# Kernel optimization log

Measured on AMD Instinct MI355X. Metric: run time of the kernel, lower is better.

Reference implementation:

```python
import jax, jax.numpy as jnp
import numpy as np

EPS = 1e-8

@jax.custom_vjp
def spike(x):
    # Heaviside forward, SuperSpike surrogate gradient in backward
    return (x > 0.0).astype(x.dtype)

def _spike_fwd(x):
    return spike(x), x

def _spike_bwd(x, g):
    return (g / (1.0 + 10.0 * jnp.abs(x)) ** 2,)

spike.defvjp(_spike_fwd, _spike_bwd)


def setup_inputs() -> dict:
    key = jax.random.key(0)
    k1, k2, k3, k4 = jax.random.split(key, 4)
    B, T, I, O = 128, 128, 1024, 1024
    x = jax.random.normal(k1, (B, T, I), dtype=jnp.float32)
    # w ~ N(0, 1/sqrt(I)) per reset_parameters
    w = jax.random.normal(k2, (I, O), dtype=jnp.float32) * np.float32(1.0 / np.sqrt(I))
    # beta ~ N(0.7, 0.01), clamped to [0,1]
    beta = jnp.clip(0.7 + 0.01 * jax.random.normal(k3, (1,), dtype=jnp.float32), 0.0, 1.0)
    # b ~ N(1.0, 0.01), clamped to >= 0
    b = jnp.clip(1.0 + 0.01 * jax.random.normal(k4, (1024,), dtype=jnp.float32), 0.0, None)
    return {"x": x, "w": w, "beta": beta, "b": b}


def reference(x, w, beta, b):
    # x: [B, T, I]; w: [I, O]; beta: [1]; b: [O]
    h = jnp.einsum('btc,cd->btd', x, w)                 # [B, T, O]
    d = jnp.einsum('ab,ac->bc', w, w)                    # lateral reset matrix [O, O]
    norm = (w ** 2).sum(0)                               # [O]
    inv_norm = 1.0 / (norm + EPS)
    B, O = x.shape[0], w.shape[1]

    def step(carry, h_t):
        mem, spk = carry
        rst = spk @ d                                    # [B, O]
        mem = (mem - rst) * beta + h_t * (1.0 - beta)
        mthr = mem * inv_norm - b
        spk = spike(mthr)
        return (mem, spk), spk

    init = (jnp.zeros((B, O), x.dtype), jnp.zeros((B, O), x.dtype))
    _, spk_rec = jax.lax.scan(step, init, jnp.swapaxes(h, 0, 1))  # [T, B, O]
    spk_rec = jnp.swapaxes(spk_rec, 0, 1)                # [B, T, O]
    loss = 0.5 * (spk_rec ** 2).mean()
    return spk_rec, loss
```

## Files before the change

### kernel.cpp

```cpp
#include <hip/hip_runtime.h>

#define B_ 128
#define T_ 128
#define I_ 1024
#define O_ 1024
#define M_ (B_*T_)
#define NOUT (M_*O_)

typedef __attribute__((ext_vector_type(8))) short short8;
typedef __attribute__((ext_vector_type(4))) float floatx4;

__device__ __forceinline__ void gld_lds16(const void* g, void* l) {
    __builtin_amdgcn_global_load_lds((const __attribute__((address_space(1))) void*)g,
                                     (__attribute__((address_space(3))) void*)l,
                                     16, 0, 0);
}

__device__ __forceinline__ void split3(float x, unsigned short& h,
                                       unsigned short& m, unsigned short& l) {
    unsigned int b0 = __float_as_uint(x);
    h = (unsigned short)(b0 >> 16);
    float r1 = x - __uint_as_float(b0 & 0xFFFF0000u);
    unsigned int b1 = __float_as_uint(r1);
    m = (unsigned short)(b1 >> 16);
    float r2 = r1 - __uint_as_float(b1 & 0xFFFF0000u);
    l = (unsigned short)(__float_as_uint(r2) >> 16);
}

__global__ __launch_bounds__(256) void split_wt(const float* __restrict__ W,
                                                unsigned short* __restrict__ WTh,
                                                unsigned short* __restrict__ WTm,
                                                unsigned short* __restrict__ WTl) {
    __shared__ float t[64][65];
    const int tid = threadIdx.x;
    const int tx = tid & 63, ty4 = tid >> 6;
    const int r0 = blockIdx.x * 64, c0 = blockIdx.y * 64;
#pragma unroll
    for (int j = 0; j < 16; ++j) {
        int row = j * 4 + ty4;
        t[row][tx] = W[(size_t)(r0 + row) * O_ + c0 + tx];
    }
    __syncthreads();
#pragma unroll
    for (int j = 0; j < 16; ++j) {
        int i = j * 4 + ty4;
        float v = t[tx][i];
        unsigned short h, m, l;
        split3(v, h, m, l);
        size_t off = (size_t)(c0 + i) * I_ + r0 + tx;
        WTh[off] = h; WTm[off] = m; WTl[off] = l;
    }
}

__global__ __launch_bounds__(256, 3) void gemm_h_split(const float* __restrict__ X,
                                                       const unsigned short* __restrict__ WTh,
                                                       const unsigned short* __restrict__ WTm,
                                                       const unsigned short* __restrict__ WTl,
                                                       float* __restrict__ H) {
    const int K = I_, N = O_;
    __shared__ float Af[128 * 32];
    __shared__ unsigned short Bs[3][128 * 32];

    const int tid = threadIdx.x;
    const int lane = tid & 63;
    const int wid = tid >> 6;
    const int wrow = wid >> 1, wcol = wid & 1;
    const int l15 = lane & 15, quad = lane >> 4;
    const int bm = blockIdx.x * 128, bn = blockIdx.y * 128;

    floatx4 acc[4][4];
#pragma unroll
    for (int mt = 0; mt < 4; ++mt)
#pragma unroll
        for (int nt = 0; nt < 4; ++nt) acc[mt][nt] = (floatx4)(0.f);

    for (int kt = 0; kt < 32; ++kt) {
        const int k0 = kt * 32;
        __syncthreads();
#pragma unroll
        for (int s = 0; s < 4; ++s) {
            int slot = tid + 256 * s;
            int row = slot >> 3, ch = slot & 7;
            gld_lds16(X + (size_t)(bm + row) * K + k0 + ch * 4, (float*)Af + (size_t)slot * 4);
        }
#pragma unroll
        for (int s = 0; s < 2; ++s) {
            int slot = tid + 256 * s;
            int col = slot >> 2, ch = slot & 3;
            size_t goff = (size_t)(bn + col) * K + k0 + ch * 8;
            gld_lds16(WTh + goff, (unsigned short*)Bs + (size_t)slot * 8);
            gld_lds16(WTm + goff, (unsigned short*)Bs + 4096 + (size_t)slot * 8);
            gld_lds16(WTl + goff, (unsigned short*)Bs + 8192 + (size_t)slot * 8);
        }
        __syncthreads();

        short8 Ah[4], Am[4], Al[4];
#pragma unroll
        for (int mt = 0; mt < 4; ++mt) {
            int row = wrow * 64 + mt * 16 + l15;
            const float* ap = (const float*)Af + row * 32 + quad * 8;
            float4 x0 = *(const float4*)(ap);
            float4 x1 = *(const float4*)(ap + 4);
            float xs[8] = {x0.x, x0.y, x0.z, x0.w, x1.x, x1.y, x1.z, x1.w};
#pragma unroll
            for (int j = 0; j < 8; ++j) {
                unsigned short hh, mm, ll;
                split3(xs[j], hh, mm, ll);
                Ah[mt][j] = (short)hh; Am[mt][j] = (short)mm; Al[mt][j] = (short)ll;
            }
        }
#pragma unroll
        for (int pb = 0; pb < 3; ++pb) {
            short8 Bf[4];
#pragma unroll
            for (int nt = 0; nt < 4; ++nt) {
                int col = wcol * 64 + nt * 16 + l15;
                Bf[nt] = *((const short8*)((const unsigned short*)Bs + pb * 4096 + col * 32 + quad * 8));
            }
#pragma unroll
            for (int nt = 0; nt < 4; ++nt)
#pragma unroll
                for (int mt = 0; mt < 4; ++mt) {
                    acc[mt][nt] = __builtin_amdgcn_mfma_f32_16x16x32_bf16(Ah[mt], Bf[nt], acc[mt][nt], 0, 0, 0);
                    acc[mt][nt] = __builtin_amdgcn_mfma_f32_16x16x32_bf16(Am[mt], Bf[nt], acc[mt][nt], 0, 0, 0);
                    if (pb < 2)
                        acc[mt][nt] = __builtin_amdgcn_mfma_f32_16x16x32_bf16(Al[mt], Bf[nt], acc[mt][nt], 0, 0, 0);
                }
        }
    }

#pragma unroll
    for (int mt = 0; mt < 4; ++mt)
#pragma unroll
        for (int nt = 0; nt < 4; ++nt) {
            int grow = bm + wrow * 64 + mt * 16 + quad * 4;
            int gcol = bn + wcol * 64 + nt * 16 + l15;
            float* hp = H + (size_t)grow * N + gcol;
#pragma unroll
            for (int r = 0; r < 4; ++r) hp[(size_t)r * N] = acc[mt][nt][r];
        }
}

__global__ __launch_bounds__(256) void gemm_wtw(const float* __restrict__ W,
                                                float* __restrict__ D) {
    const int K = I_, N = O_;
    __shared__ float As[32][68];
    __shared__ float Bs[32][68];
    const int tid = threadIdx.x;
    const int tx = tid & 15, ty = tid >> 4;
    const int bj = blockIdx.x * 64, bo = blockIdx.y * 64;
    const int lr = tid >> 4;
    const int lc = (tid & 15) << 2;

    float acc[4][4];
#pragma unroll
    for (int m = 0; m < 4; m++)
#pragma unroll
        for (int n = 0; n < 4; n++) acc[m][n] = 0.f;

    for (int k0 = 0; k0 < K; k0 += 32) {
        float4 a0 = *(const float4*)(W + (size_t)(k0 + lr) * N + bj + lc);
        float4 a1 = *(const float4*)(W + (size_t)(k0 + lr + 16) * N + bj + lc);
        float4 b0 = *(const float4*)(W + (size_t)(k0 + lr) * N + bo + lc);
        float4 b1 = *(const float4*)(W + (size_t)(k0 + lr + 16) * N + bo + lc);
        __syncthreads();
        *(float4*)&As[lr][lc] = a0; *(float4*)&As[lr + 16][lc] = a1;
        *(float4*)&Bs[lr][lc] = b0; *(float4*)&Bs[lr + 16][lc] = b1;
        __syncthreads();
#pragma unroll
        for (int k = 0; k < 32; ++k) {
            float4 av = *(const float4*)&As[k][ty * 4];
            float4 bv = *(const float4*)&Bs[k][tx * 4];
            float am[4] = {av.x, av.y, av.z, av.w};
            float bb[4] = {bv.x, bv.y, bv.z, bv.w};
#pragma unroll
            for (int m = 0; m < 4; m++)
#pragma unroll
                for (int n = 0; n < 4; n++) acc[m][n] += am[m] * bb[n];
        }
    }
#pragma unroll
    for (int m = 0; m < 4; m++) {
        float4 v = make_float4(acc[m][0], acc[m][1], acc[m][2], acc[m][3]);
        *(float4*)(D + (size_t)(bj + ty * 4 + m) * N + bo + tx * 4) = v;
    }
}

__global__ void colnorm_diag(const float* __restrict__ D, float* __restrict__ invn,
                             unsigned int* __restrict__ counter) {
    int o = blockIdx.x * 256 + threadIdx.x;
    if (o == 0) *counter = 0u;
    invn[o] = 1.0f / (D[(size_t)o * O_ + o] + 1e-8f);
}

__global__ __launch_bounds__(256) void scan_kernel(const float* __restrict__ h,
                                                   const float* __restrict__ d,
                                                   const float* __restrict__ invn,
                                                   const float* __restrict__ bias,
                                                   const float* __restrict__ beta,
                                                   float* __restrict__ out,
                                                   unsigned int* __restrict__ spike_count) {
    __shared__ int lst[2][O_];
    __shared__ int cnt[2];
    __shared__ unsigned int red[256];

    const int tid = threadIdx.x;
    const int lane = tid & 63;
    const int b = blockIdx.x;
    const int o4 = tid * 4;
    const float betav = beta[0];
    const float omb = 1.0f - betav;

    const float4 invn4 = *(const float4*)(invn + o4);
    const float4 b4 = *(const float4*)(bias + o4);
    float4 mem4 = make_float4(0.f, 0.f, 0.f, 0.f);

    if (tid < 2) cnt[tid] = 0;
    unsigned int local_count = 0;
    const float* hb = h + (size_t)b * T_ * O_;
    float* ob = out + (size_t)b * T_ * O_;
    const unsigned long long below = (lane == 63) ? 0xFFFFFFFFFFFFFFFFull >> 1
                                                  : ((1ull << lane) - 1ull);

    float4 hcur = *(const float4*)(hb + o4);
    __syncthreads();

    for (int t = 0; t < T_; ++t) {
        const int p = t & 1, q = p ^ 1;
        const int n = cnt[p];
        __syncthreads();
        if (tid == 0) cnt[p] = 0;

        float4 hnext = make_float4(0.f, 0.f, 0.f, 0.f);
        if (t + 1 < T_) hnext = *(const float4*)(hb + (size_t)(t + 1) * O_ + o4);

        float4 rst = make_float4(0.f, 0.f, 0.f, 0.f);
        int i = 0;
        for (; i + 16 <= n; i += 16) {
            float4 v[16];
#pragma unroll
            for (int u = 0; u < 16; ++u) {
                const int j = lst[p][i + u];
                v[u] = *(const float4*)(d + (size_t)j * O_ + o4);
            }
#pragma unroll
            for (int u = 0; u < 16; ++u) {
                rst.x += v[u].x; rst.y += v[u].y;
                rst.z += v[u].z; rst.w += v[u].w;
            }
        }
        for (; i + 4 <= n; i += 4) {
            float4 v[4];
#pragma unroll
            for (int u = 0; u < 4; ++u) {
                const int j = lst[p][i + u];
                v[u] = *(const float4*)(d + (size_t)j * O_ + o4);
            }
#pragma unroll
            for (int u = 0; u < 4; ++u) {
                rst.x += v[u].x; rst.y += v[u].y;
                rst.z += v[u].z; rst.w += v[u].w;
            }
        }
        for (; i < n; ++i) {
            const int j = lst[p][i];
            float4 v = *(const float4*)(d + (size_t)j * O_ + o4);
            rst.x += v.x; rst.y += v.y; rst.z += v.z; rst.w += v.w;
        }

        mem4.x = (mem4.x - rst.x) * betav + hcur.x * omb;
        mem4.y = (mem4.y - rst.y) * betav + hcur.y * omb;
        mem4.z = (mem4.z - rst.z) * betav + hcur.z * omb;
        mem4.w = (mem4.w - rst.w) * betav + hcur.w * omb;

        const int s[4] = {(mem4.x * invn4.x - b4.x) > 0.0f,
                          (mem4.y * invn4.y - b4.y) > 0.0f,
                          (mem4.z * invn4.z - b4.z) > 0.0f,
                          (mem4.w * invn4.w - b4.w) > 0.0f};

        float4 sv = make_float4(s[0] ? 1.f : 0.f, s[1] ? 1.f : 0.f,
                                s[2] ? 1.f : 0.f, s[3] ? 1.f : 0.f);
        *(float4*)(ob + (size_t)t * O_ + o4) = sv;
        local_count += (unsigned)(s[0] + s[1] + s[2] + s[3]);

#pragma unroll
        for (int u = 0; u < 4; ++u) {
            unsigned long long mask = __ballot(s[u]);
            int base = 0;
            if (lane == 0 && mask) base = atomicAdd(&cnt[q], __popcll(mask));
            base = __shfl(base, 0, 64);
            if (s[u]) lst[q][base + __popcll(mask & below)] = o4 + u;
        }

        __syncthreads();
        hcur = hnext;
    }

    red[tid] = local_count;
    __syncthreads();
    for (int st = 128; st > 0; st >>= 1) {
        if (tid < st) red[tid] += red[tid + st];
        __syncthreads();
    }
    if (tid == 0) atomicAdd(spike_count, red[0]);
}

__global__ void finalize_loss(const unsigned int* __restrict__ spike_count,
                              float* __restrict__ loss_out) {
    *loss_out = 0.5f * ((float)(*spike_count) / 16777216.0f);
}

extern "C" void kernel_launch(void* const* d_in, const int* in_sizes, int n_in,
                              void* d_out, int out_size, void* d_ws, size_t ws_size,
                              hipStream_t stream) {
    const float* x    = (const float*)d_in[0];
    const float* w    = (const float*)d_in[1];
    const float* beta = (const float*)d_in[2];
    const float* bias = (const float*)d_in[3];
    float* out = (float*)d_out;

    char* ws = (char*)d_ws;
    float* h    = (float*)ws;
    float* dmat = (float*)(ws + (size_t)67108864);
    float* invn = (float*)(ws + (size_t)71303168);
    unsigned int* cntp = (unsigned int*)(ws + (size_t)71307264);
    unsigned short* wt_h = (unsigned short*)(ws + (size_t)71311360);
    unsigned short* wt_m = (unsigned short*)(ws + (size_t)73408512);
    unsigned short* wt_l = (unsigned short*)(ws + (size_t)75505664);

    split_wt<<<dim3(I_ / 64, O_ / 64), 256, 0, stream>>>(w, wt_h, wt_m, wt_l);
    gemm_h_split<<<dim3(M_ / 128, O_ / 128), 256, 0, stream>>>(x, wt_h, wt_m, wt_l, h);
    gemm_wtw<<<dim3(O_ / 64, O_ / 64), 256, 0, stream>>>(w, dmat);
    colnorm_diag<<<O_ / 256, 256, 0, stream>>>(dmat, invn, cntp);
    scan_kernel<<<B_, 256, 0, stream>>>(h, dmat, invn, bias, beta, out, cntp);
    finalize_loss<<<1, 1, 0, stream>>>(cntp, out + (size_t)NOUT);
}
```

Before: 555.7 us.

## Pre-split X into bf16 triples and swizzle LDS tiles in the GEMM

```diff
diff --git a/kernel.cpp b/kernel.cpp
--- a/kernel.cpp
+++ b/kernel.cpp
@@ -27,6 +27,22 @@
     l = (unsigned short)(__float_as_uint(r2) >> 16);
 }
 
+__global__ __launch_bounds__(256) void split_x(const float* __restrict__ X,
+                                               unsigned short* __restrict__ Xh,
+                                               unsigned short* __restrict__ Xm,
+                                               unsigned short* __restrict__ Xl) {
+    size_t base = ((size_t)blockIdx.x * 256 + threadIdx.x) * 4;
+    float4 v = *(const float4*)(X + base);
+    ushort4 hh, mm, ll;
+    split3(v.x, hh.x, mm.x, ll.x);
+    split3(v.y, hh.y, mm.y, ll.y);
+    split3(v.z, hh.z, mm.z, ll.z);
+    split3(v.w, hh.w, mm.w, ll.w);
+    *(ushort4*)(Xh + base) = hh;
+    *(ushort4*)(Xm + base) = mm;
+    *(ushort4*)(Xl + base) = ll;
+}
+
 __global__ __launch_bounds__(256) void split_wt(const float* __restrict__ W,
                                                 unsigned short* __restrict__ WTh,
                                                 unsigned short* __restrict__ WTm,
@@ -52,14 +68,13 @@
     }
 }
 
-__global__ __launch_bounds__(256, 3) void gemm_h_split(const float* __restrict__ X,
-                                                       const unsigned short* __restrict__ WTh,
-                                                       const unsigned short* __restrict__ WTm,
-                                                       const unsigned short* __restrict__ WTl,
-                                                       float* __restrict__ H) {
+__global__ __launch_bounds__(256, 3) void gemm_h_mfma(
+        const unsigned short* __restrict__ Xh, const unsigned short* __restrict__ Xm,
+        const unsigned short* __restrict__ Xl, const unsigned short* __restrict__ WTh,
+        const unsigned short* __restrict__ WTm, const unsigned short* __restrict__ WTl,
+        float* __restrict__ H) {
     const int K = I_, N = O_;
-    __shared__ float Af[128 * 32];
-    __shared__ unsigned short Bs[3][128 * 32];
+    __shared__ unsigned short P[6][128 * 32];
 
     const int tid = threadIdx.x;
     const int lane = tid & 63;
@@ -68,6 +83,16 @@
     const int l15 = lane & 15, quad = lane >> 4;
     const int bm = blockIdx.x * 128, bn = blockIdx.y * 128;
 
+    const int srow = tid >> 2, sch = tid & 3;
+    const int schg = sch ^ ((srow >> 1) & 3);
+    const unsigned short* gsrc[6];
+    gsrc[0] = Xh  + (size_t)(bm + srow) * K + schg * 8;
+    gsrc[1] = Xm  + (size_t)(bm + srow) * K + schg * 8;
+    gsrc[2] = Xl  + (size_t)(bm + srow) * K + schg * 8;
+    gsrc[3] = WTh + (size_t)(bn + srow) * K + schg * 8;
+    gsrc[4] = WTm + (size_t)(bn + srow) * K + schg * 8;
+    gsrc[5] = WTl + (size_t)(bn + srow) * K + schg * 8;
+
     floatx4 acc[4][4];
 #pragma unroll
     for (int mt = 0; mt < 4; ++mt)
@@ -78,53 +103,39 @@
         const int k0 = kt * 32;
         __syncthreads();
 #pragma unroll
-        for (int s = 0; s < 4; ++s) {
-            int slot = tid + 256 * s;
-            int row = slot >> 3, ch = slot & 7;
-            gld_lds16(X + (size_t)(bm + row) * K + k0 + ch * 4, (float*)Af + (size_t)slot * 4);
-        }
-#pragma unroll
-        for (int s = 0; s < 2; ++s) {
-            int slot = tid + 256 * s;
-            int col = slot >> 2, ch = slot & 3;
-            size_t goff = (size_t)(bn + col) * K + k0 + ch * 8;
-            gld_lds16(WTh + goff, (unsigned short*)Bs + (size_t)slot * 8);
-            gld_lds16(WTm + goff, (unsigned short*)Bs + 4096 + (size_t)slot * 8);
-            gld_lds16(WTl + goff, (unsigned short*)Bs + 8192 + (size_t)slot * 8);
-        }
-        __syncthreads();
-
-        short8 Ah[4], Am[4], Al[4];
-#pragma unroll
-        for (int mt = 0; mt < 4; ++mt) {
-            int row = wrow * 64 + mt * 16 + l15;
-            const float* ap = (const float*)Af + row * 32 + quad * 8;
-            float4 x0 = *(const float4*)(ap);
-            float4 x1 = *(const float4*)(ap + 4);
-            float xs[8] = {x0.x, x0.y, x0.z, x0.w, x1.x, x1.y, x1.z, x1.w};
-#pragma unroll
-            for (int j = 0; j < 8; ++j) {
-                unsigned short hh, mm, ll;
-                split3(xs[j], hh, mm, ll);
-                Ah[mt][j] = (short)hh; Am[mt][j] = (short)mm; Al[mt][j] = (short)ll;
-            }
-        }
+        for (int p = 0; p < 6; ++p) {
+            unsigned short* dst = (unsigned short*)P + p * 4096 + tid * 8;
+            gld_lds16(gsrc[p] + k0, dst);
+            gld_lds16(gsrc[p] + (size_t)64 * K + k0, dst + 2048);
+        }
+        __syncthreads();
+
+        short8 Af[3][4];
+#pragma unroll
+        for (int pa = 0; pa < 3; ++pa)
+#pragma unroll
+            for (int mt = 0; mt < 4; ++mt) {
+                int row = wrow * 64 + mt * 16 + l15;
+                int chk = quad ^ ((row >> 1) & 3);
+                Af[pa][mt] = *(const short8*)((const unsigned short*)P + pa * 4096 + row * 32 + chk * 8);
+            }
 #pragma unroll
         for (int pb = 0; pb < 3; ++pb) {
             short8 Bf[4];
 #pragma unroll
             for (int nt = 0; nt < 4; ++nt) {
                 int col = wcol * 64 + nt * 16 + l15;
-                Bf[nt] = *((const short8*)((const unsigned short*)Bs + pb * 4096 + col * 32 + quad * 8));
+                int chk = quad ^ ((col >> 1) & 3);
+                Bf[nt] = *(const short8*)((const unsigned short*)P + (3 + pb) * 4096 + col * 32 + chk * 8);
             }
 #pragma unroll
             for (int nt = 0; nt < 4; ++nt)
 #pragma unroll
                 for (int mt = 0; mt < 4; ++mt) {
-                    acc[mt][nt] = __builtin_amdgcn_mfma_f32_16x16x32_bf16(Ah[mt], Bf[nt], acc[mt][nt], 0, 0, 0);
-                    acc[mt][nt] = __builtin_amdgcn_mfma_f32_16x16x32_bf16(Am[mt], Bf[nt], acc[mt][nt], 0, 0, 0);
+                    acc[mt][nt] = __builtin_amdgcn_mfma_f32_16x16x32_bf16(Af[0][mt], Bf[nt], acc[mt][nt], 0, 0, 0);
+                    acc[mt][nt] = __builtin_amdgcn_mfma_f32_16x16x32_bf16(Af[1][mt], Bf[nt], acc[mt][nt], 0, 0, 0);
                     if (pb < 2)
-                        acc[mt][nt] = __builtin_amdgcn_mfma_f32_16x16x32_bf16(Al[mt], Bf[nt], acc[mt][nt], 0, 0, 0);
+                        acc[mt][nt] = __builtin_amdgcn_mfma_f32_16x16x32_bf16(Af[2][mt], Bf[nt], acc[mt][nt], 0, 0, 0);
                 }
         }
     }
@@ -327,9 +338,14 @@
     unsigned short* wt_h = (unsigned short*)(ws + (size_t)71311360);
     unsigned short* wt_m = (unsigned short*)(ws + (size_t)73408512);
     unsigned short* wt_l = (unsigned short*)(ws + (size_t)75505664);
-
+    unsigned short* x_h  = (unsigned short*)(ws + (size_t)77602816);
+    unsigned short* x_m  = (unsigned short*)(ws + (size_t)111157248);
+    unsigned short* x_l  = (unsigned short*)(ws + (size_t)144711680);
+
+    split_x<<<M_ * I_ / 1024, 256, 0, stream>>>(x, x_h, x_m, x_l);
     split_wt<<<dim3(I_ / 64, O_ / 64), 256, 0, stream>>>(w, wt_h, wt_m, wt_l);
-    gemm_h_split<<<dim3(M_ / 128, O_ / 128), 256, 0, stream>>>(x, wt_h, wt_m, wt_l, h);
+    gemm_h_mfma<<<dim3(M_ / 128, O_ / 128), 256, 0, stream>>>(x_h, x_m, x_l,
+                                                              wt_h, wt_m, wt_l, h);
     gemm_wtw<<<dim3(O_ / 64, O_ / 64), 256, 0, stream>>>(w, dmat);
     colnorm_diag<<<O_ / 256, 256, 0, stream>>>(dmat, invn, cntp);
     scan_kernel<<<B_, 256, 0, stream>>>(h, dmat, invn, bias, beta, out, cntp);
```

Result: faster. 538.1 us (-3.2%).
